# Kernel optimization log

Measured on AMD Instinct MI355X. Metric: run time of the kernel, lower is better.

The kernel has to match this reference:

```python
import jax, jax.numpy as jnp
import numpy as np

B, T, D, R = 8, 4096, 1024, 1024
INIT = 0.02

def setup_inputs() -> dict:
    key = jax.random.key(0)
    ks = jax.random.split(key, 8)
    x = jax.random.normal(ks[0], (B, T, D), dtype=jnp.float32)
    attention_mask = jnp.ones((B, T), dtype=bool)
    W_Q = jax.random.normal(ks[1], (D, D), dtype=jnp.float32) * (1.0 / np.sqrt(D))
    W_K = jax.random.normal(ks[2], (D, D), dtype=jnp.float32) * (1.0 / np.sqrt(D))
    U = jax.random.normal(ks[3], (D, R), dtype=jnp.float32) * INIT
    V = jax.random.normal(ks[4], (D, R), dtype=jnp.float32) * INIT
    Wb = jax.random.normal(ks[5], (D, R), dtype=jnp.float32) * INIT
    bias = jnp.zeros((D,), dtype=jnp.float32)
    W_O = jax.random.normal(ks[6], (D, D), dtype=jnp.float32) * (1.0 / np.sqrt(D))
    return {"x": x, "attention_mask": attention_mask, "W_Q": W_Q, "W_K": W_K,
            "U": U, "V": V, "Wb": Wb, "bias": bias, "W_O": W_O}

def reference(x, attention_mask, W_Q, W_K, U, V, Wb, bias, W_O):
    # Q = x @ W_Q^T, K = x @ W_K^T  (torch Linear stores weight as (out,in))
    Q = jnp.einsum('btd,ed->bte', x, W_Q)
    K = jnp.einsum('btd,ed->bte', x, W_K)
    m = attention_mask.astype(x.dtype)               # (B,T)
    A = Q @ V                                        # (B,T,R)  = Q_i V
    Kw = (K @ Wb) * m[..., None]                     # pad-masked K_j W
    S = jnp.cumsum(Kw, axis=1)                       # causal prefix sum over j<=i
    n = jnp.cumsum(m, axis=1)[..., None]             # n_valid per i, (B,T,1)
    # sum_{j<=i} BCN(Q_i,K_j) = ((Q_iV) * S_i) U^T + n_i * bias; then divide by max(n_i,1)
    out = ((A * S) @ U.T + n * bias) / jnp.clip(n, 1.0)
    return jnp.einsum('btd,ed->bte', out, W_O)
```

## Files before the change

### kernel.cpp

```cpp
#include <hip/hip_runtime.h>
#include <hip/hip_bf16.h>

typedef __attribute__((ext_vector_type(8))) short short8;
typedef __attribute__((ext_vector_type(4))) float f32x4;

#define Bc 8
#define Tc 4096
#define Dc 1024
#define Rc 1024
#define BT (Bc*Tc)

__device__ inline float b2f(ushort u) {
    union { float f; unsigned int i; } x; x.i = ((unsigned int)u) << 16; return x.f;
}
__device__ inline ushort f2b(float f) {
    union { float f; unsigned int i; } x; x.f = f;
    unsigned int r = x.i + 0x7fffu + ((x.i >> 16) & 1u);
    return (ushort)(r >> 16);
}

__device__ inline void gload16(const void* g, void* l) {
    __builtin_amdgcn_global_load_lds(
        (const __attribute__((address_space(1))) unsigned int*)g,
        (__attribute__((address_space(3))) unsigned int*)l, 16, 0, 0);
}


__device__ __attribute__((always_inline)) inline
short8 lds_frag(const char* mat, int rowbase, int k, int fr, int hi) {
    const int row = rowbase + fr;
    const int byte = (row << 7) + (((k << 6) + (hi << 4)) ^ ((row & 7) << 4));
    return *(const short8*)(mat + byte);
}

template<int KK>
__device__ __attribute__((always_inline)) inline
void rdb(const char* BB, short8 (&bf)[2][4], int wn, int fr, int hi) {
#pragma unroll
    for (int n = 0; n < 4; ++n)
        bf[KK][n] = lds_frag(BB, (wn << 6) + (n << 4), KK, fr, hi);
}

template<int MQ, int KK>
__device__ __attribute__((always_inline)) inline
void rda(const char* AB, short8 (&af)[4], int wm, int fr, int hi) {
#pragma unroll
    for (int i = 0; i < 4; ++i)
        af[i] = lds_frag(AB, (wm << 7) + ((MQ * 4 + i) << 4), KK, fr, hi);
}

template<int MQ, int KK>
__device__ __attribute__((always_inline)) inline
void mmq(f32x4 (&acc)[8][4], const short8 (&af)[4], const short8 (&bf)[2][4]) {
#pragma unroll
    for (int i = 0; i < 4; ++i)
#pragma unroll
        for (int n = 0; n < 4; ++n)
            acc[MQ * 4 + i][n] = __builtin_amdgcn_mfma_f32_16x16x32_bf16(
                af[i], bf[KK][n], acc[MQ * 4 + i][n], 0, 0, 0);
}

#define PH_MID do { __builtin_amdgcn_sched_barrier(0); __builtin_amdgcn_s_barrier(); \
    __builtin_amdgcn_s_setprio(1); } while (0)
#define PH_END do { __builtin_amdgcn_s_setprio(0); __builtin_amdgcn_sched_barrier(0); \
    __builtin_amdgcn_s_barrier(); } while (0)

#define STG(G, ld, thr, grow0, gk, lbase) do { \
    const ushort* _p = (G) + (size_t)(grow0) * (ld) + (gk); \
    gload16(_p + (thr), (lbase) + thrD); \
    gload16(_p + (size_t)64 * (ld) + (thr), (lbase) + thrD + 8192); } while (0)

#define TILE(cAb, cBb, stA, stB, tn, tn2) do { \
     \
    rdb<0>(cBb, bf, wn, fr, hi); \
    rda<0, 0>(cAb, afA, wm, fr, hi); \
    rda<1, 0>(cAb, afB, wm, fr, hi); \
    STG(Ab, lda, thrA, m0, (tn) << 6, stA); \
    PH_MID; mmq<0, 0>(acc, afA, bf); PH_END; \
     \
    rdb<1>(cBb, bf, wn, fr, hi); \
    rda<0, 1>(cAb, afA, wm, fr, hi); \
    STG(Ab, lda, thrA, m0 + 128, (tn) << 6, stA + 16384); \
    PH_MID; mmq<1, 0>(acc, afB, bf); PH_END; \
     \
    rda<1, 1>(cAb, afB, wm, fr, hi); \
    PH_MID; mmq<0, 1>(acc, afA, bf); PH_END; \
     \
    STG(Bt, ldb, thrB, n0,       (tn2) << 6, stB); \
    STG(Bt, ldb, thrB, n0 + 128, (tn2) << 6, stB + 16384); \
    PH_MID; mmq<1, 1>(acc, afB, bf); \
    __builtin_amdgcn_s_setprio(0); __builtin_amdgcn_sched_barrier(0); \
    asm volatile("s_waitcnt vmcnt(4)" ::: "memory"); \
    __builtin_amdgcn_s_barrier(); } while (0)

template<int EPI, int DOCS>
__global__ __launch_bounds__(512, 2)
void gemm256(const ushort* __restrict__ Ab, const ushort* __restrict__ Bt,
             void* __restrict__ Cout, const float* __restrict__ bias,
             const float* __restrict__ maskf, float* __restrict__ csum,
             int ntx, int K, int lda, int ldb, int ldc) {
    __shared__ __align__(16) char sA[65536];
    __shared__ __align__(16) char sB[65536];

    const int tid = threadIdx.x;
    const int w = tid >> 6, l = tid & 63;
    const int wm = w >> 2, wn = w & 3;
    const int fr = l & 15, hi = l >> 4;
    const int srow = (w << 3) + (l >> 3);
    const int scg = (((l & 7) ^ (l >> 3)) << 3);
    const size_t thrA = (size_t)srow * lda + scg;
    const size_t thrB = (size_t)srow * ldb + scg;
    const int thrD = (w << 10) + (l << 4);

    const int nwg = (int)gridDim.x;
    const int q = nwg >> 3;
    const int bid = (int)blockIdx.x;
    const int swz = (bid & 7) * q + (bid >> 3);
    const int by = swz / ntx, bx = swz % ntx;
    const int m0 = by << 8, n0 = bx << 8;

    f32x4 acc[8][4] = {};
    short8 afA[4], afB[4], bf[2][4];
    const int NT = K >> 6;

    STG(Ab, lda, thrA, m0,        0,  sA);
    STG(Ab, lda, thrA, m0 + 128,  0,  sA + 16384);
    STG(Bt, ldb, thrB, n0,        0,  sB);
    STG(Bt, ldb, thrB, n0 + 128,  0,  sB + 16384);
    STG(Bt, ldb, thrB, n0,        64, sB + 32768);
    STG(Bt, ldb, thrB, n0 + 128,  64, sB + 32768 + 16384);
    asm volatile("s_waitcnt vmcnt(4)" ::: "memory");
    __builtin_amdgcn_sched_barrier(0);
    __builtin_amdgcn_s_barrier();

    const char* cA0 = sA;
    const char* cB0 = sB;
    const char* cA1 = sA + 32768;
    const char* cB1 = sB + 32768;

    for (int it = 0; it < (NT >> 1); ++it) {
        const int t1 = 2 * it + 1;
        const int t2 = min(2 * it + 2, NT - 1);
        const int t3 = min(2 * it + 3, NT - 1);
        TILE(cA0, cB0, sA + 32768, sB, t1, t2);
        TILE(cA1, cB1, sA, sB + 32768, t2, t3);
    }

    const int crow = m0 + (wm << 7);
    const int ccol = n0 + (wn << 6);
#pragma unroll
    for (int m = 0; m < 8; ++m) {
#pragma unroll
        for (int n = 0; n < 4; ++n) {
            const int r0 = crow + (m << 4) + (hi << 2);
            const int c = ccol + (n << 4) + fr;
            if (EPI == 0) {
                ushort* C = (ushort*)Cout;
#pragma unroll
                for (int t = 0; t < 4; ++t)
                    C[(size_t)(r0 + t) * ldc + c] = f2b(acc[m][n][t]);
            } else {
                float* C = (float*)Cout;
                const float bv = bias[c];
#pragma unroll
                for (int t = 0; t < 4; ++t)
                    C[(size_t)(r0 + t) * ldc + c] = acc[m][n][t] + bv;
            }
        }
    }

    if (DOCS && n0 >= 1024) {
        const float* mrow = maskf + crow;
#pragma unroll
        for (int mh = 0; mh < 2; ++mh) {
            float cs0 = 0.f, cs1 = 0.f, cs2 = 0.f, cs3 = 0.f;
#pragma unroll
            for (int mm = 0; mm < 4; ++mm) {
                const int m = mh * 4 + mm;
                const float4 mk = *(const float4*)(mrow + (m << 4) + (hi << 2));
                cs0 += acc[m][0][0] * mk.x + acc[m][0][1] * mk.y + acc[m][0][2] * mk.z + acc[m][0][3] * mk.w;
                cs1 += acc[m][1][0] * mk.x + acc[m][1][1] * mk.y + acc[m][1][2] * mk.z + acc[m][1][3] * mk.w;
                cs2 += acc[m][2][0] * mk.x + acc[m][2][1] * mk.y + acc[m][2][2] * mk.z + acc[m][2][3] * mk.w;
                cs3 += acc[m][3][0] * mk.x + acc[m][3][1] * mk.y + acc[m][3][2] * mk.z + acc[m][3][3] * mk.w;
            }
            float cs[4] = {cs0, cs1, cs2, cs3};
            const int g = (crow + (mh << 6)) >> 6;
#pragma unroll
            for (int n = 0; n < 4; ++n) {
                float v = cs[n];
                v += __shfl_xor(v, 16, 64);
                v += __shfl_xor(v, 32, 64);
                if (hi == 0) {
                    const int r = (ccol - 1024) + (n << 4) + fr;
                    csum[(size_t)g * 1024 + r] = v;
                }
            }
        }
    }
}

__global__ void cast_f32_bf16(const float4* __restrict__ in, ushort4* __restrict__ out, int n4) {
    int i = blockIdx.x * blockDim.x + threadIdx.x;
    int stride = gridDim.x * blockDim.x;
    for (; i < n4; i += stride) {
        float4 v = in[i];
        ushort4 o;
        o.x = f2b(v.x); o.y = f2b(v.y); o.z = f2b(v.z); o.w = f2b(v.w);
        out[i] = o;
    }
}

__global__ void prep_weights(const float* __restrict__ V,  const float* __restrict__ Wb,
                             const float* __restrict__ U,  const float* __restrict__ WQ,
                             const float* __restrict__ WK, const float* __restrict__ WO,
                             ushort* __restrict__ Vt,  ushort* __restrict__ Wbt,
                             ushort* __restrict__ Ut,  ushort* __restrict__ WQt,
                             ushort* __restrict__ WKt, ushort* __restrict__ WOb) {
    __shared__ float tile[32][33];
    const float* in; ushort* out;
    switch (blockIdx.z) {
        case 0: in = V;  out = Vt;  break;
        case 1: in = Wb; out = Wbt; break;
        case 2: in = U;  out = Ut;  break;
        case 3: in = WQ; out = WQt; break;
        case 4: in = WK; out = WKt; break;
        default: in = WO; out = WOb; break;
    }
    int c0 = blockIdx.x * 32, r0 = blockIdx.y * 32;
    int tx = threadIdx.x & 31, ty = threadIdx.x >> 5;
    if (blockIdx.z < 5) {
        for (int i = 0; i < 32; i += 8)
            tile[ty + i][tx] = in[(size_t)(r0 + ty + i) * 1024 + c0 + tx];
        __syncthreads();
        for (int i = 0; i < 32; i += 8)
            out[(size_t)(c0 + ty + i) * 1024 + r0 + tx] = f2b(tile[tx][ty + i]);
    } else {
        for (int i = 0; i < 32; i += 8)
            out[(size_t)(r0 + ty + i) * 1024 + c0 + tx] =
                f2b(in[(size_t)(r0 + ty + i) * 1024 + c0 + tx]);
    }
}

__global__ __launch_bounds__(256)
void gemm_bt3(const ushort* __restrict__ Vt,  const ushort* __restrict__ WQt,
              const ushort* __restrict__ Wbt, const ushort* __restrict__ WKt,
              const ushort* __restrict__ WOb, const ushort* __restrict__ Ut,
              ushort* __restrict__ W1, ushort* __restrict__ Mmat) {
    const ushort *A, *Bt; ushort* Cout;
    switch (blockIdx.z) {
        case 0: A = Vt;  Bt = WQt; Cout = W1; break;
        case 1: A = Wbt; Bt = WKt; Cout = W1 + (size_t)Rc * Dc; break;
        default: A = WOb; Bt = Ut; Cout = Mmat; break;
    }
    __shared__ __align__(16) ushort As[128][32];
    __shared__ __align__(16) ushort Bs[128][32];
    const int tid = threadIdx.x;
    const int wave = tid >> 6, lane = tid & 63;
    const int m0 = blockIdx.y * 128, n0 = blockIdx.x * 128;
    const int wr = (wave >> 1) * 64, wc = (wave & 1) * 64;

    f32x4 acc[4][4] = {};

    const int rS = wave * 32 + (lane >> 2);
    const int kS = (lane & 3) * 8;
    const int fr = lane & 15;
    const int fq = (lane >> 4) * 8;

    for (int kt = 0; kt < 32; ++kt) {
        const int k0 = kt << 5;
        __syncthreads();
        gload16(A  + (size_t)(m0 + rS) * 1024      + k0 + kS, &As[rS][kS]);
        gload16(A  + (size_t)(m0 + rS + 16) * 1024 + k0 + kS, &As[rS + 16][kS]);
        gload16(Bt + (size_t)(n0 + rS) * 1024      + k0 + kS, &Bs[rS][kS]);
        gload16(Bt + (size_t)(n0 + rS + 16) * 1024 + k0 + kS, &Bs[rS + 16][kS]);
        __syncthreads();

        short8 af[4], bfr[4];
        #pragma unroll
        for (int i = 0; i < 4; i++) af[i]  = *(const short8*)&As[wr + i * 16 + fr][fq];
        #pragma unroll
        for (int i = 0; i < 4; i++) bfr[i] = *(const short8*)&Bs[wc + i * 16 + fr][fq];
        #pragma unroll
        for (int i = 0; i < 4; i++)
            #pragma unroll
            for (int j = 0; j < 4; j++)
                acc[i][j] = __builtin_amdgcn_mfma_f32_16x16x32_bf16(af[i], bfr[j], acc[i][j], 0, 0, 0);
    }

    const int rq = (lane >> 4) * 4;
    #pragma unroll
    for (int i = 0; i < 4; i++) {
        #pragma unroll
        for (int j = 0; j < 4; j++) {
            int row = m0 + wr + i * 16 + rq;
            int col = n0 + wc + j * 16 + fr;
            #pragma unroll
            for (int t = 0; t < 4; t++)
                Cout[(size_t)(row + t) * 1024 + col] = f2b(acc[i][j][t]);
        }
    }
}

__global__ void bias_O_kernel(const float* __restrict__ W_O, const float* __restrict__ bias,
                              float* __restrict__ biasO) {
    __shared__ float sh[256];
    int e = blockIdx.x, tid = threadIdx.x;
    float s = 0.f;
    for (int d = tid; d < Dc; d += 256) s += W_O[(size_t)e * Dc + d] * bias[d];
    sh[tid] = s; __syncthreads();
    for (int o = 128; o > 0; o >>= 1) { if (tid < o) sh[tid] += sh[tid + o]; __syncthreads(); }
    if (tid == 0) biasO[e] = sh[0];
}

__global__ void mask_scan(const int* __restrict__ mask, float* __restrict__ nbuf,
                          float* __restrict__ maskf) {
    __shared__ float sh[256];
    int b = blockIdx.x, tid = threadIdx.x;
    float run = 0.f;
    for (int t0 = 0; t0 < Tc; t0 += 256) {
        float v = (mask[b * Tc + t0 + tid] != 0) ? 1.f : 0.f;
        maskf[b * Tc + t0 + tid] = v;
        sh[tid] = v; __syncthreads();
        for (int off = 1; off < 256; off <<= 1) {
            float add = (tid >= off) ? sh[tid - off] : 0.f;
            __syncthreads();
            sh[tid] += add;
            __syncthreads();
        }
        nbuf[b * Tc + t0 + tid] = run + sh[tid];
        run += sh[255];
        __syncthreads();
    }
}

#define NCHUNK 64
#define LCHUNK (Tc / NCHUNK)

__global__ void scan_apply(ushort* __restrict__ AKw, const int* __restrict__ mask,
                           const float* __restrict__ csum, const float* __restrict__ nbuf) {
    const int r = threadIdx.x * 4;
    const int chunk = blockIdx.x, b = blockIdx.y;
    const int row0 = b * Tc + chunk * LCHUNK;
    float4 s = {0.f, 0.f, 0.f, 0.f};
    for (int c = 0; c < chunk; ++c) {
        float4 v = *(const float4*)(csum + (((size_t)b * NCHUNK + c) << 10) + r);
        s.x += v.x; s.y += v.y; s.z += v.z; s.w += v.w;
    }
    ushort* p = AKw + (size_t)row0 * 2048 + r;
    for (int t = 0; t < LCHUNK; ++t) {
        const size_t off = (size_t)t * 2048;
        if (mask[row0 + t] != 0) {
            ushort4 kw = *(const ushort4*)(p + off + 1024);
            s.x += b2f(kw.x); s.y += b2f(kw.y); s.z += b2f(kw.z); s.w += b2f(kw.w);
        }
        const float rn = 1.f / fmaxf(nbuf[row0 + t], 1.f);
        ushort4 a = *(const ushort4*)(p + off);
        ushort4 o;
        o.x = f2b(b2f(a.x) * s.x * rn);
        o.y = f2b(b2f(a.y) * s.y * rn);
        o.z = f2b(b2f(a.z) * s.z * rn);
        o.w = f2b(b2f(a.w) * s.w * rn);
        *(ushort4*)(p + off) = o;
    }
}

extern "C" void kernel_launch(void* const* d_in, const int* in_sizes, int n_in,
                              void* d_out, int out_size, void* d_ws, size_t ws_size,
                              hipStream_t stream) {
    const float* x    = (const float*)d_in[0];
    const int*   mask = (const int*)d_in[1];
    const float* W_Q  = (const float*)d_in[2];
    const float* W_K  = (const float*)d_in[3];
    const float* U    = (const float*)d_in[4];
    const float* V    = (const float*)d_in[5];
    const float* Wb   = (const float*)d_in[6];
    const float* bias = (const float*)d_in[7];
    const float* W_O  = (const float*)d_in[8];
    float* out = (float*)d_out;

    char* ws = (char*)d_ws;
    ushort* xb   = (ushort*)ws; ws += (size_t)BT * Dc * 2;
    ushort* AKw  = (ushort*)ws; ws += (size_t)BT * 2048 * 2;
    ushort* W1   = (ushort*)ws; ws += (size_t)2048 * Dc * 2;
    ushort* Mmat = (ushort*)ws; ws += (size_t)Dc * Rc * 2;
    ushort* Vt   = (ushort*)ws; ws += (size_t)Dc * Rc * 2;
    ushort* Wbt  = (ushort*)ws; ws += (size_t)Dc * Rc * 2;
    ushort* Ut   = (ushort*)ws; ws += (size_t)Dc * Rc * 2;
    ushort* WQt  = (ushort*)ws; ws += (size_t)Dc * Dc * 2;
    ushort* WKt  = (ushort*)ws; ws += (size_t)Dc * Dc * 2;
    ushort* WOb  = (ushort*)ws; ws += (size_t)Dc * Dc * 2;
    float*  csum = (float*)ws;  ws += (size_t)Bc * NCHUNK * Rc * 4;
    float*  nbuf = (float*)ws;  ws += (size_t)Bc * Tc * 4;
    float*  maskf= (float*)ws;  ws += (size_t)Bc * Tc * 4;
    float*  biasO = (float*)ws; ws += (size_t)Dc * 4;

    cast_f32_bf16<<<2048, 256, 0, stream>>>((const float4*)x, (ushort4*)xb, BT * Dc / 4);
    prep_weights<<<dim3(32, 32, 6), 256, 0, stream>>>(V, Wb, U, W_Q, W_K, W_O,
                                                      Vt, Wbt, Ut, WQt, WKt, WOb);
    mask_scan<<<Bc, 256, 0, stream>>>(mask, nbuf, maskf);

    gemm_bt3<<<dim3(8, 8, 3), 256, 0, stream>>>(Vt, WQt, Wbt, WKt, WOb, Ut, W1, Mmat);
    bias_O_kernel<<<Dc, 256, 0, stream>>>(W_O, bias, biasO);

    gemm256<0, 1><<<1024, 512, 0, stream>>>(xb, W1, AKw, nullptr, maskf, csum,
                                            8, Dc, Dc, Dc, 2048);

    scan_apply<<<dim3(NCHUNK, Bc), 256, 0, stream>>>(AKw, mask, csum, nbuf);

    gemm256<1, 0><<<512, 512, 0, stream>>>(AKw, Mmat, out, biasO, nullptr, nullptr,
                                           4, Rc, 2048, Rc, Dc);
}
```

Before: 394.0 us.

## Make GEMM blocks persistent over several N tiles with cross-tile prefetch

Each GEMM workgroup now computes NTILES consecutive 256-wide output tiles along N instead of one, with the grid shrunk to 256 blocks. The last two K-steps of each tile prefetch the first K-slices of the next tile's B, and A is reloaded from K=0, so the pipeline stays full across tiles. The goal is to amortize prologue and epilogue costs and cut launch tail effects. In exchange, 256 blocks at 2 per CU leaves some CUs underused on a 256-CU part, and each epilogue stalls the pipeline.

```diff
diff --git a/kernel.cpp b/kernel.cpp
--- a/kernel.cpp
+++ b/kernel.cpp
@@ -70,30 +70,30 @@
     gload16(_p + (thr), (lbase) + thrD); \
     gload16(_p + (size_t)64 * (ld) + (thr), (lbase) + thrD + 8192); } while (0)
 
-#define TILE(cAb, cBb, stA, stB, tn, tn2) do { \
+#define TILE2(cAb, cBb, stA, stB, tnA, nB, tnB) do { \
      \
     rdb<0>(cBb, bf, wn, fr, hi); \
     rda<0, 0>(cAb, afA, wm, fr, hi); \
     rda<1, 0>(cAb, afB, wm, fr, hi); \
-    STG(Ab, lda, thrA, m0, (tn) << 6, stA); \
+    STG(Ab, lda, thrA, m0, (tnA) << 6, stA); \
     PH_MID; mmq<0, 0>(acc, afA, bf); PH_END; \
      \
     rdb<1>(cBb, bf, wn, fr, hi); \
     rda<0, 1>(cAb, afA, wm, fr, hi); \
-    STG(Ab, lda, thrA, m0 + 128, (tn) << 6, stA + 16384); \
+    STG(Ab, lda, thrA, m0 + 128, (tnA) << 6, stA + 16384); \
     PH_MID; mmq<1, 0>(acc, afB, bf); PH_END; \
      \
     rda<1, 1>(cAb, afB, wm, fr, hi); \
     PH_MID; mmq<0, 1>(acc, afA, bf); PH_END; \
      \
-    STG(Bt, ldb, thrB, n0,       (tn2) << 6, stB); \
-    STG(Bt, ldb, thrB, n0 + 128, (tn2) << 6, stB + 16384); \
+    STG(Bt, ldb, thrB, (nB),       (tnB) << 6, stB); \
+    STG(Bt, ldb, thrB, (nB) + 128, (tnB) << 6, stB + 16384); \
     PH_MID; mmq<1, 1>(acc, afB, bf); \
     __builtin_amdgcn_s_setprio(0); __builtin_amdgcn_sched_barrier(0); \
     asm volatile("s_waitcnt vmcnt(4)" ::: "memory"); \
     __builtin_amdgcn_s_barrier(); } while (0)
 
-template<int EPI, int DOCS>
+template<int EPI, int DOCS, int NTILES>
 __global__ __launch_bounds__(512, 2)
 void gemm256(const ushort* __restrict__ Ab, const ushort* __restrict__ Bt,
              void* __restrict__ Cout, const float* __restrict__ bias,
@@ -116,12 +116,20 @@
     const int q = nwg >> 3;
     const int bid = (int)blockIdx.x;
     const int swz = (bid & 7) * q + (bid >> 3);
-    const int by = swz / ntx, bx = swz % ntx;
-    const int m0 = by << 8, n0 = bx << 8;
-
-    f32x4 acc[8][4] = {};
+    const int xpb = ntx / NTILES;
+    const int by = swz / xpb, sub = swz % xpb;
+    const int m0 = by << 8;
+
+    f32x4 acc[8][4];
     short8 afA[4], afB[4], bf[2][4];
     const int NT = K >> 6;
+
+    const char* cA0 = sA;
+    const char* cB0 = sB;
+    const char* cA1 = sA + 32768;
+    const char* cB1 = sB + 32768;
+
+    int n0 = (sub * NTILES) << 8;
 
     STG(Ab, lda, thrA, m0,        0,  sA);
     STG(Ab, lda, thrA, m0 + 128,  0,  sA + 16384);
@@ -133,69 +141,76 @@
     __builtin_amdgcn_sched_barrier(0);
     __builtin_amdgcn_s_barrier();
 
-    const char* cA0 = sA;
-    const char* cB0 = sB;
-    const char* cA1 = sA + 32768;
-    const char* cB1 = sB + 32768;
-
-    for (int it = 0; it < (NT >> 1); ++it) {
-        const int t1 = 2 * it + 1;
-        const int t2 = min(2 * it + 2, NT - 1);
-        const int t3 = min(2 * it + 3, NT - 1);
-        TILE(cA0, cB0, sA + 32768, sB, t1, t2);
-        TILE(cA1, cB1, sA, sB + 32768, t2, t3);
-    }
-
-    const int crow = m0 + (wm << 7);
-    const int ccol = n0 + (wn << 6);
-#pragma unroll
-    for (int m = 0; m < 8; ++m) {
-#pragma unroll
-        for (int n = 0; n < 4; ++n) {
-            const int r0 = crow + (m << 4) + (hi << 2);
-            const int c = ccol + (n << 4) + fr;
-            if (EPI == 0) {
-                ushort* C = (ushort*)Cout;
-#pragma unroll
-                for (int t = 0; t < 4; ++t)
-                    C[(size_t)(r0 + t) * ldc + c] = f2b(acc[m][n][t]);
-            } else {
-                float* C = (float*)Cout;
-                const float bv = bias[c];
-#pragma unroll
-                for (int t = 0; t < 4; ++t)
-                    C[(size_t)(r0 + t) * ldc + c] = acc[m][n][t] + bv;
-            }
-        }
-    }
-
-    if (DOCS && n0 >= 1024) {
-        const float* mrow = maskf + crow;
-#pragma unroll
-        for (int mh = 0; mh < 2; ++mh) {
-            float cs0 = 0.f, cs1 = 0.f, cs2 = 0.f, cs3 = 0.f;
-#pragma unroll
-            for (int mm = 0; mm < 4; ++mm) {
-                const int m = mh * 4 + mm;
-                const float4 mk = *(const float4*)(mrow + (m << 4) + (hi << 2));
-                cs0 += acc[m][0][0] * mk.x + acc[m][0][1] * mk.y + acc[m][0][2] * mk.z + acc[m][0][3] * mk.w;
-                cs1 += acc[m][1][0] * mk.x + acc[m][1][1] * mk.y + acc[m][1][2] * mk.z + acc[m][1][3] * mk.w;
-                cs2 += acc[m][2][0] * mk.x + acc[m][2][1] * mk.y + acc[m][2][2] * mk.z + acc[m][2][3] * mk.w;
-                cs3 += acc[m][3][0] * mk.x + acc[m][3][1] * mk.y + acc[m][3][2] * mk.z + acc[m][3][3] * mk.w;
-            }
-            float cs[4] = {cs0, cs1, cs2, cs3};
-            const int g = (crow + (mh << 6)) >> 6;
+    for (int tt = 0; tt < NTILES; ++tt) {
+        const int n0n = (tt + 1 < NTILES) ? n0 + 256 : n0;
+
+#pragma unroll
+        for (int m = 0; m < 8; ++m)
+#pragma unroll
+            for (int n = 0; n < 4; ++n)
+                acc[m][n] = (f32x4){0.f, 0.f, 0.f, 0.f};
+
+        for (int it = 0; it < (NT >> 1) - 1; ++it) {
+            const int t1 = 2 * it + 1, t2 = 2 * it + 2, t3 = 2 * it + 3;
+            TILE2(cA0, cB0, sA + 32768, sB,         t1, n0, t2);
+            TILE2(cA1, cB1, sA,         sB + 32768, t2, n0, t3);
+        }
+        TILE2(cA0, cB0, sA + 32768, sB,         NT - 1, n0n, 0);
+        TILE2(cA1, cB1, sA,         sB + 32768, 0,      n0n, 1);
+
+        const int crow = m0 + (wm << 7);
+        const int ccol = n0 + (wn << 6);
+#pragma unroll
+        for (int m = 0; m < 8; ++m) {
 #pragma unroll
             for (int n = 0; n < 4; ++n) {
-                float v = cs[n];
-                v += __shfl_xor(v, 16, 64);
-                v += __shfl_xor(v, 32, 64);
-                if (hi == 0) {
-                    const int r = (ccol - 1024) + (n << 4) + fr;
-                    csum[(size_t)g * 1024 + r] = v;
+                const int r0 = crow + (m << 4) + (hi << 2);
+                const int c = ccol + (n << 4) + fr;
+                if (EPI == 0) {
+                    ushort* C = (ushort*)Cout;
+#pragma unroll
+                    for (int t = 0; t < 4; ++t)
+                        C[(size_t)(r0 + t) * ldc + c] = f2b(acc[m][n][t]);
+                } else {
+                    float* C = (float*)Cout;
+                    const float bv = bias[c];
+#pragma unroll
+                    for (int t = 0; t < 4; ++t)
+                        C[(size_t)(r0 + t) * ldc + c] = acc[m][n][t] + bv;
                 }
             }
         }
+
+        if (DOCS && n0 >= 1024) {
+            const float* mrow = maskf + crow;
+#pragma unroll
+            for (int mh = 0; mh < 2; ++mh) {
+                float cs0 = 0.f, cs1 = 0.f, cs2 = 0.f, cs3 = 0.f;
+#pragma unroll
+                for (int mm = 0; mm < 4; ++mm) {
+                    const int m = mh * 4 + mm;
+                    const float4 mk = *(const float4*)(mrow + (m << 4) + (hi << 2));
+                    cs0 += acc[m][0][0] * mk.x + acc[m][0][1] * mk.y + acc[m][0][2] * mk.z + acc[m][0][3] * mk.w;
+                    cs1 += acc[m][1][0] * mk.x + acc[m][1][1] * mk.y + acc[m][1][2] * mk.z + acc[m][1][3] * mk.w;
+                    cs2 += acc[m][2][0] * mk.x + acc[m][2][1] * mk.y + acc[m][2][2] * mk.z + acc[m][2][3] * mk.w;
+                    cs3 += acc[m][3][0] * mk.x + acc[m][3][1] * mk.y + acc[m][3][2] * mk.z + acc[m][3][3] * mk.w;
+                }
+                float cs[4] = {cs0, cs1, cs2, cs3};
+                const int g = (crow + (mh << 6)) >> 6;
+#pragma unroll
+                for (int n = 0; n < 4; ++n) {
+                    float v = cs[n];
+                    v += __shfl_xor(v, 16, 64);
+                    v += __shfl_xor(v, 32, 64);
+                    if (hi == 0) {
+                        const int r = (ccol - 1024) + (n << 4) + fr;
+                        csum[(size_t)g * 1024 + r] = v;
+                    }
+                }
+            }
+        }
+
+        n0 = n0n;
     }
 }
 
@@ -402,11 +417,11 @@
     gemm_bt3<<<dim3(8, 8, 3), 256, 0, stream>>>(Vt, WQt, Wbt, WKt, WOb, Ut, W1, Mmat);
     bias_O_kernel<<<Dc, 256, 0, stream>>>(W_O, bias, biasO);
 
-    gemm256<0, 1><<<1024, 512, 0, stream>>>(xb, W1, AKw, nullptr, maskf, csum,
-                                            8, Dc, Dc, Dc, 2048);
+    gemm256<0, 1, 4><<<256, 512, 0, stream>>>(xb, W1, AKw, nullptr, maskf, csum,
+                                              8, Dc, Dc, Dc, 2048);
 
     scan_apply<<<dim3(NCHUNK, Bc), 256, 0, stream>>>(AKw, mask, csum, nbuf);
 
-    gemm256<1, 0><<<512, 512, 0, stream>>>(AKw, Mmat, out, biasO, nullptr, nullptr,
-                                           4, Rc, 2048, Rc, Dc);
-}
+    gemm256<1, 0, 2><<<256, 512, 0, stream>>>(AKw, Mmat, out, biasO, nullptr, nullptr,
+                                              4, Rc, 2048, Rc, Dc);
+}
```

New measurement: 505.4 us. 1.28x slower.
